# Optimization experiments

Measured on AMD Instinct MI355X. Metric: run time of the kernel, lower is better.

Reference implementation:

```python
import jax, jax.numpy as jnp
from jax import lax
import numpy as np

B, T, IN, H, OUT = 64, 512, 128, 512, 1


def _lstm_layer(x, W_ih, W_hh, b_ih, b_hh):
    # x: [B, T, in]; W_ih: [4H, in]; W_hh: [4H, H]; biases: [4H]
    # PyTorch gate order: i, f, g, o
    xg = jnp.einsum('bti,gi->btg', x, W_ih) + (b_ih + b_hh)  # [B, T, 4H]
    Hd = W_hh.shape[1]
    h0 = jnp.zeros((x.shape[0], Hd), x.dtype)

    def step(carry, xt):
        h, c = carry
        g = xt + h @ W_hh.T  # [B, 4H]
        i, f, gg, o = jnp.split(g, 4, axis=-1)
        i = jax.nn.sigmoid(i)
        f = jax.nn.sigmoid(f)
        gg = jnp.tanh(gg)
        o = jax.nn.sigmoid(o)
        c = f * c + i * gg
        h = o * jnp.tanh(c)
        return (h, c), h

    (_, _), hs = lax.scan(step, (h0, h0), jnp.swapaxes(xg, 0, 1))  # hs: [T, B, H]
    return jnp.swapaxes(hs, 0, 1)  # [B, T, H]


def setup_inputs() -> dict:
    key = jax.random.key(0)
    ks = jax.random.split(key, 11)
    s_in = 1.0 / np.sqrt(H)
    inp = {
        'x': jax.random.normal(ks[0], (B, T, IN), jnp.float32),
        'W_ih0': jax.random.uniform(ks[1], (4 * H, IN), jnp.float32, -s_in, s_in),
        'W_hh0': jax.random.uniform(ks[2], (4 * H, H), jnp.float32, -s_in, s_in),
        'b_ih0': jax.random.uniform(ks[3], (4 * H,), jnp.float32, -s_in, s_in),
        'b_hh0': jax.random.uniform(ks[4], (4 * H,), jnp.float32, -s_in, s_in),
        'W_ih1': jax.random.uniform(ks[5], (4 * H, H), jnp.float32, -s_in, s_in),
        'W_hh1': jax.random.uniform(ks[6], (4 * H, H), jnp.float32, -s_in, s_in),
        'b_ih1': jax.random.uniform(ks[7], (4 * H,), jnp.float32, -s_in, s_in),
        'b_hh1': jax.random.uniform(ks[8], (4 * H,), jnp.float32, -s_in, s_in),
        'Wl': jax.random.uniform(ks[9], (OUT, H), jnp.float32, -s_in, s_in),
        'bl': jax.random.uniform(ks[10], (OUT,), jnp.float32, -s_in, s_in),
    }
    return inp


def reference(x, W_ih0, W_hh0, b_ih0, b_hh0, W_ih1, W_hh1, b_ih1, b_hh1, Wl, bl):
    h = _lstm_layer(x, W_ih0, W_hh0, b_ih0, b_hh0)   # layer 0
    h = _lstm_layer(h, W_ih1, W_hh1, b_ih1, b_hh1)   # layer 1
    last = h[:, -1, :]                                # [B, H]
    out = last @ Wl.T + bl                            # [B, OUT]; classification=False -> no sigmoid
    return out
```

## Files before the change

### kernel.cpp

```cpp
#include <hip/hip_runtime.h>
#include <cmath>

#define TT 512
#define BB 64
#define HH 512
#define II 128
#define NBLK 256

typedef float v2f __attribute__((ext_vector_type(2)));
__device__ __forceinline__ v2f fma2(v2f a, v2f b, v2f c) { return __builtin_elementwise_fma(a, b, c); }

#define SMEM_FLOATS (16384 + 16384 + 1024 + 256 + 16)
#define SMEM_BYTES  (SMEM_FLOATS * 4)

__device__ __forceinline__ float sigm(float v) { return 1.0f / (1.0f + expf(-v)); }
__device__ __forceinline__ unsigned umin2(unsigned a, unsigned b) { return a < b ? a : b; }
#define CBAR() asm volatile("" ::: "memory")

__device__ __forceinline__ void step(const float* wk, float v, v2f (&acc)[8]) {
  const float4* wp = (const float4*)wk;
  const float4 w0 = wp[0], w1 = wp[1], w2 = wp[2], w3 = wp[3];
  const v2f vb = (v2f){v, v};
  acc[0] = fma2((v2f){w0.x, w0.y}, vb, acc[0]);
  acc[1] = fma2((v2f){w0.z, w0.w}, vb, acc[1]);
  acc[2] = fma2((v2f){w1.x, w1.y}, vb, acc[2]);
  acc[3] = fma2((v2f){w1.z, w1.w}, vb, acc[3]);
  acc[4] = fma2((v2f){w2.x, w2.y}, vb, acc[4]);
  acc[5] = fma2((v2f){w2.z, w2.w}, vb, acc[5]);
  acc[6] = fma2((v2f){w3.x, w3.y}, vb, acc[6]);
  acc[7] = fma2((v2f){w3.z, w3.w}, vb, acc[7]);
}

template<int KN>
__device__ __forceinline__ void loadva(const float* __restrict__ src, int k0,
                                       int b, float (&v)[KN]) {
#pragma unroll
  for (int i = 0; i < KN; ++i)
    v[i] = __hip_atomic_load(src + (size_t)(k0 + i) * BB + b,
                             __ATOMIC_RELAXED, __HIP_MEMORY_SCOPE_AGENT);
}
template<int KN>
__device__ __forceinline__ void loadv(const float* __restrict__ src, int k0,
                                      int b, float (&v)[KN]) {
#pragma unroll
  for (int i = 0; i < KN; ++i) v[i] = src[(size_t)(k0 + i) * BB + b];
}
template<int KN>
__device__ __forceinline__ void consume(const float* __restrict__ wbase, int k0,
                                        const float (&v)[KN], v2f (&acc)[8]) {
#pragma unroll
  for (int i = 0; i < KN; ++i) step(wbase + (size_t)(k0 + i) * 16, v[i], acc);
}

__device__ __forceinline__ void span32(const float* __restrict__ src,
                                       const float* __restrict__ wbase,
                                       int k0, int b, v2f (&acc)[8]) {
  float va[8], vb_[8];
  loadva<8>(src, k0, b, va);
  loadva<8>(src, k0 + 8, b, vb_);
  consume<8>(wbase, k0, va, acc);
  loadva<8>(src, k0 + 16, b, va);
  consume<8>(wbase, k0 + 8, vb_, acc);
  loadva<8>(src, k0 + 24, b, vb_);
  consume<8>(wbase, k0 + 16, va, acc);
  consume<8>(wbase, k0 + 24, vb_, acc);
}

__global__ __launch_bounds__(1024) void k_transpose_x(const float* __restrict__ x,
                                                      float* __restrict__ xT) {
  __shared__ float tile[64][65];
  const int t  = blockIdx.x >> 1;
  const int k0 = (blockIdx.x & 1) << 6;
  const int lk = threadIdx.x & 63;
  const int lb = threadIdx.x >> 6;
#pragma unroll
  for (int bp = 0; bp < 64; bp += 16) {
    const int b = bp + lb;
    tile[lk][b] = x[((size_t)b * TT + t) * II + k0 + lk];
  }
  __syncthreads();
  const int b2  = threadIdx.x & 63;
  const int kk0 = threadIdx.x >> 6;
#pragma unroll
  for (int kp = 0; kp < 64; kp += 16) {
    const int kk = kp + kk0;
    xT[((size_t)t * II + k0 + kk) * BB + b2] = tile[kk][b2];
  }
}

__global__ void k_init_flags(unsigned* flags) { flags[threadIdx.x] = 0u; }

__global__ __launch_bounds__(1024, 4) void k_lstm_persist(
    const float* __restrict__ xT,
    const float* __restrict__ W_ih0, const float* __restrict__ W_hh0,
    const float* __restrict__ b_ih0, const float* __restrict__ b_hh0,
    const float* __restrict__ W_ih1, const float* __restrict__ W_hh1,
    const float* __restrict__ b_ih1, const float* __restrict__ b_hh1,
    float* __restrict__ h0ring, float* __restrict__ h1ring,
    unsigned* __restrict__ flags)
{
  extern __shared__ float smem[];
  float* wlds  = smem;
  float* part  = wlds + 16384;
  float* gates = part + 16384;
  float* cst   = gates + 1024;
  float* bsum  = cst + 256;

  const int bid = blockIdx.x;
  const int L   = bid >> 7;
  const int ub  = (bid & 127) << 2;
  const int tid = threadIdx.x;

  const float* WA = L ? W_ih1 : W_ih0;
  const float* WB = L ? W_hh1 : W_hh0;
  const int KA = L ? HH : II;

  const int ktot = KA + HH;
  for (int idx = tid; idx < 16 * ktot; idx += 1024) {
    const int k  = idx >> 4;
    const int lr = idx & 15;
    const int u = lr >> 2, q = lr & 3;
    const int G = q * HH + ub + u;
    wlds[idx] = (k < KA) ? WA[G * KA + k] : WB[G * HH + (k - KA)];
  }
  if (tid < 16) {
    const int u = tid >> 2, q = tid & 3;
    const int G = q * HH + ub + u;
    bsum[tid] = L ? (b_ih1[G] + b_hh1[G]) : (b_ih0[G] + b_hh0[G]);
  }
  if (tid < 256) cst[tid] = 0.0f;
  __syncthreads();

  const int kseg = tid >> 6;
  const int b    = tid & 63;

  for (int s = 0; s <= TT; ++s) {
    const int t = L ? (s - 1) : s;
    const bool active = (t >= 0 && t < TT);
    const bool first  = (t == 0);

    v2f acc[8];
#pragma unroll
    for (int j = 0; j < 8; ++j) acc[j] = (v2f){0.0f, 0.0f};

    float xv[8];
    if (active && L == 0) {
      loadv<8>(xT + (size_t)t * (II * BB), kseg * 8, b, xv);
    }

    if (s > 0) {
      if (tid < 64) {
        const unsigned tgt = (unsigned)s;
        for (;;) {
          const unsigned m0 = __hip_atomic_load(flags + tid,       __ATOMIC_RELAXED, __HIP_MEMORY_SCOPE_AGENT);
          const unsigned m1 = __hip_atomic_load(flags + tid +  64, __ATOMIC_RELAXED, __HIP_MEMORY_SCOPE_AGENT);
          const unsigned m2 = __hip_atomic_load(flags + tid + 128, __ATOMIC_RELAXED, __HIP_MEMORY_SCOPE_AGENT);
          const unsigned m3 = __hip_atomic_load(flags + tid + 192, __ATOMIC_RELAXED, __HIP_MEMORY_SCOPE_AGENT);
          const unsigned mn = umin2(umin2(m0, m1), umin2(m2, m3));
          if (__all(mn >= tgt)) break;
          __builtin_amdgcn_s_sleep(1);
        }
      }
      __syncthreads();
      CBAR();
    }

    if (active) {
      if (L == 0) {
        consume<8>(wlds, kseg * 8, xv, acc);
        if (!first) {
          span32(h0ring + (size_t)((s - 1) & 1) * (HH * BB),
                 wlds + (size_t)II * 16, kseg * 32, b, acc);
        }
      } else {
        const float* h0p = h0ring + (size_t)((s - 1) & 1) * (HH * BB);
        span32(h0p, wlds, kseg * 32, b, acc);
        if (!first) {
          span32(h1ring + (size_t)(s & 1) * (HH * BB),
                 wlds + (size_t)HH * 16, kseg * 32, b, acc);
        }
      }

#pragma unroll
      for (int j = 0; j < 4; ++j) {
        part[(((j << 2) + 0) * 16 + kseg) * 64 + b] = acc[(j << 1)].x;
        part[(((j << 2) + 1) * 16 + kseg) * 64 + b] = acc[(j << 1)].y;
        part[(((j << 2) + 2) * 16 + kseg) * 64 + b] = acc[(j << 1) + 1].x;
        part[(((j << 2) + 3) * 16 + kseg) * 64 + b] = acc[(j << 1) + 1].y;
      }
      __syncthreads();
      {
        const int row = tid >> 6;
        const int bb  = tid & 63;
        float g = 0.0f;
#pragma unroll
        for (int ks = 0; ks < 16; ++ks) g += part[(row * 16 + ks) * 64 + bb];
        gates[row * 64 + bb] = g + bsum[row];
      }
      __syncthreads();

      if (tid < 256) {
        const int u = tid >> 6, bb = tid & 63;
        const float gi = sigm(gates[((u << 2) + 0) * 64 + bb]);
        const float gf = sigm(gates[((u << 2) + 1) * 64 + bb]);
        const float gg = tanhf(gates[((u << 2) + 2) * 64 + bb]);
        const float go = sigm(gates[((u << 2) + 3) * 64 + bb]);
        const float cold = first ? 0.0f : cst[u * 64 + bb];
        const float cn = gf * cold + gi * gg;
        const float hn = go * tanhf(cn);
        cst[u * 64 + bb] = cn;
        float* hdst = (L ? h1ring : h0ring) + (size_t)(t & 1) * (HH * BB);
        float old = __hip_atomic_exchange(hdst + (ub + u) * 64 + bb, hn,
                                          __ATOMIC_RELAXED, __HIP_MEMORY_SCOPE_AGENT);
        asm volatile("" :: "v"(old));
      }
    }

    __syncthreads();
    if (tid == 0) {
      __hip_atomic_store(flags + bid, (unsigned)(s + 1),
                         __ATOMIC_RELAXED, __HIP_MEMORY_SCOPE_AGENT);
    }
  }
}

__global__ __launch_bounds__(512) void k_final(const float* __restrict__ h1last,
                                               const float* __restrict__ Wl,
                                               const float* __restrict__ bl,
                                               float* __restrict__ out) {
  __shared__ float red[8][64];
  const int jg = threadIdx.x >> 6, b = threadIdx.x & 63;
  float a = 0.0f;
  for (int jj = 0; jj < 64; ++jj) {
    const int j = (jg << 6) + jj;
    a += h1last[j * BB + b] * Wl[j];
  }
  red[jg][b] = a;
  __syncthreads();
  if (threadIdx.x < 64) {
    float s = bl[0];
#pragma unroll
    for (int g = 0; g < 8; ++g) s += red[g][threadIdx.x];
    out[threadIdx.x] = s;
  }
}

extern "C" void kernel_launch(void* const* d_in, const int* in_sizes, int n_in,
                              void* d_out, int out_size, void* d_ws, size_t ws_size,
                              hipStream_t stream) {
  (void)in_sizes; (void)n_in; (void)out_size; (void)ws_size;
  const float* x     = (const float*)d_in[0];
  const float* W_ih0 = (const float*)d_in[1];
  const float* W_hh0 = (const float*)d_in[2];
  const float* b_ih0 = (const float*)d_in[3];
  const float* b_hh0 = (const float*)d_in[4];
  const float* W_ih1 = (const float*)d_in[5];
  const float* W_hh1 = (const float*)d_in[6];
  const float* b_ih1 = (const float*)d_in[7];
  const float* b_hh1 = (const float*)d_in[8];
  const float* Wl    = (const float*)d_in[9];
  const float* bl    = (const float*)d_in[10];
  float* out = (float*)d_out;

  float* ws       = (float*)d_ws;
  float* xT       = ws;
  float* h0ring   = xT + (size_t)TT * II * BB;
  float* h1ring   = h0ring + 2 * HH * BB;
  unsigned* flags = (unsigned*)(h1ring + 2 * HH * BB);

  k_transpose_x<<<1024, 1024, 0, stream>>>(x, xT);
  k_init_flags<<<1, NBLK, 0, stream>>>(flags);

  hipFuncSetAttribute((const void*)k_lstm_persist,
                      hipFuncAttributeMaxDynamicSharedMemorySize, SMEM_BYTES);

  void* args[] = {
    (void*)&xT,
    (void*)&W_ih0, (void*)&W_hh0, (void*)&b_ih0, (void*)&b_hh0,
    (void*)&W_ih1, (void*)&W_hh1, (void*)&b_ih1, (void*)&b_hh1,
    (void*)&h0ring, (void*)&h1ring, (void*)&flags,
  };
  hipLaunchCooperativeKernel((void*)k_lstm_persist, dim3(NBLK), dim3(1024),
                             args, SMEM_BYTES, stream);

  k_final<<<1, 512, 0, stream>>>(h1ring + HH * BB, Wl, bl, out);
}
```

Baseline: 7.520 ms.

## Decouple LSTM layer sync with per-layer flags and a deeper hidden-state ring

Replaces the single all-blocks-at-step-s barrier with separate flag arrays for layer 0 and layer 1. Layer 1 now runs two steps behind layer 0, and each layer waits on its own layer for step s but only on the other layer for step s-1. The hidden-state rings grow from 2 to 4 slots so that one step of slack between layers cannot overwrite data that is still being read. The aim is to let the two layers drift slightly, so a slow block in one layer does not stall the other every step. The cost is one extra pipeline step and a larger ring footprint.

```diff
diff --git a/kernel.cpp b/kernel.cpp
--- a/kernel.cpp
+++ b/kernel.cpp
@@ -6,6 +6,7 @@
 #define HH 512
 #define II 128
 #define NBLK 256
+#define RD 4
 
 typedef float v2f __attribute__((ext_vector_type(2)));
 __device__ __forceinline__ v2f fma2(v2f a, v2f b, v2f c) { return __builtin_elementwise_fma(a, b, c); }
@@ -97,7 +98,7 @@
     const float* __restrict__ W_ih1, const float* __restrict__ W_hh1,
     const float* __restrict__ b_ih1, const float* __restrict__ b_hh1,
     float* __restrict__ h0ring, float* __restrict__ h1ring,
-    unsigned* __restrict__ flags)
+    unsigned* __restrict__ flag0, unsigned* __restrict__ flag1)
 {
   extern __shared__ float smem[];
   float* wlds  = smem;
@@ -134,8 +135,10 @@
   const int kseg = tid >> 6;
   const int b    = tid & 63;
 
-  for (int s = 0; s <= TT; ++s) {
-    const int t = L ? (s - 1) : s;
+  const int SMAX = TT + 2;
+
+  for (int s = 0; s < SMAX; ++s) {
+    const int t = L ? (s - 2) : s;
     const bool active = (t >= 0 && t < TT);
     const bool first  = (t == 0);
 
@@ -150,14 +153,15 @@
 
     if (s > 0) {
       if (tid < 64) {
-        const unsigned tgt = (unsigned)s;
+        const unsigned tA = L ? (unsigned)(s - 1) : (unsigned)s;
+        const unsigned tB = L ? (unsigned)s : (unsigned)(s - 1);
         for (;;) {
-          const unsigned m0 = __hip_atomic_load(flags + tid,       __ATOMIC_RELAXED, __HIP_MEMORY_SCOPE_AGENT);
-          const unsigned m1 = __hip_atomic_load(flags + tid +  64, __ATOMIC_RELAXED, __HIP_MEMORY_SCOPE_AGENT);
-          const unsigned m2 = __hip_atomic_load(flags + tid + 128, __ATOMIC_RELAXED, __HIP_MEMORY_SCOPE_AGENT);
-          const unsigned m3 = __hip_atomic_load(flags + tid + 192, __ATOMIC_RELAXED, __HIP_MEMORY_SCOPE_AGENT);
-          const unsigned mn = umin2(umin2(m0, m1), umin2(m2, m3));
-          if (__all(mn >= tgt)) break;
+          const unsigned a0 = __hip_atomic_load(flag0 + tid,      __ATOMIC_RELAXED, __HIP_MEMORY_SCOPE_AGENT);
+          const unsigned a1 = __hip_atomic_load(flag0 + tid + 64, __ATOMIC_RELAXED, __HIP_MEMORY_SCOPE_AGENT);
+          const unsigned b0 = __hip_atomic_load(flag1 + tid,      __ATOMIC_RELAXED, __HIP_MEMORY_SCOPE_AGENT);
+          const unsigned b1 = __hip_atomic_load(flag1 + tid + 64, __ATOMIC_RELAXED, __HIP_MEMORY_SCOPE_AGENT);
+          const bool ok = (umin2(a0, a1) >= tA) && (umin2(b0, b1) >= tB);
+          if (__all(ok)) break;
           __builtin_amdgcn_s_sleep(1);
         }
       }
@@ -169,14 +173,14 @@
       if (L == 0) {
         consume<8>(wlds, kseg * 8, xv, acc);
         if (!first) {
-          span32(h0ring + (size_t)((s - 1) & 1) * (HH * BB),
+          span32(h0ring + (size_t)((s - 1) & 3) * (HH * BB),
                  wlds + (size_t)II * 16, kseg * 32, b, acc);
         }
       } else {
-        const float* h0p = h0ring + (size_t)((s - 1) & 1) * (HH * BB);
-        span32(h0p, wlds, kseg * 32, b, acc);
+        span32(h0ring + (size_t)((s - 2) & 3) * (HH * BB), wlds,
+               kseg * 32, b, acc);
         if (!first) {
-          span32(h1ring + (size_t)(s & 1) * (HH * BB),
+          span32(h1ring + (size_t)((s - 3) & 3) * (HH * BB),
                  wlds + (size_t)HH * 16, kseg * 32, b, acc);
         }
       }
@@ -209,7 +213,7 @@
         const float cn = gf * cold + gi * gg;
         const float hn = go * tanhf(cn);
         cst[u * 64 + bb] = cn;
-        float* hdst = (L ? h1ring : h0ring) + (size_t)(t & 1) * (HH * BB);
+        float* hdst = (L ? h1ring : h0ring) + (size_t)(t & 3) * (HH * BB);
         float old = __hip_atomic_exchange(hdst + (ub + u) * 64 + bb, hn,
                                           __ATOMIC_RELAXED, __HIP_MEMORY_SCOPE_AGENT);
         asm volatile("" :: "v"(old));
@@ -218,7 +222,8 @@
 
     __syncthreads();
     if (tid == 0) {
-      __hip_atomic_store(flags + bid, (unsigned)(s + 1),
+      unsigned* fl = (L ? flag1 : flag0) + (bid & 127);
+      __hip_atomic_store(fl, (unsigned)(s + 1),
                          __ATOMIC_RELAXED, __HIP_MEMORY_SCOPE_AGENT);
     }
   }
@@ -265,11 +270,12 @@
   float* ws       = (float*)d_ws;
   float* xT       = ws;
   float* h0ring   = xT + (size_t)TT * II * BB;
-  float* h1ring   = h0ring + 2 * HH * BB;
-  unsigned* flags = (unsigned*)(h1ring + 2 * HH * BB);
+  float* h1ring   = h0ring + (size_t)RD * HH * BB;
+  unsigned* flag0 = (unsigned*)(h1ring + (size_t)RD * HH * BB);
+  unsigned* flag1 = flag0 + 128;
 
   k_transpose_x<<<1024, 1024, 0, stream>>>(x, xT);
-  k_init_flags<<<1, NBLK, 0, stream>>>(flags);
+  k_init_flags<<<1, NBLK, 0, stream>>>(flag0);
 
   hipFuncSetAttribute((const void*)k_lstm_persist,
                       hipFuncAttributeMaxDynamicSharedMemorySize, SMEM_BYTES);
@@ -278,10 +284,11 @@
     (void*)&xT,
     (void*)&W_ih0, (void*)&W_hh0, (void*)&b_ih0, (void*)&b_hh0,
     (void*)&W_ih1, (void*)&W_hh1, (void*)&b_ih1, (void*)&b_hh1,
-    (void*)&h0ring, (void*)&h1ring, (void*)&flags,
+    (void*)&h0ring, (void*)&h1ring, (void*)&flag0, (void*)&flag1,
   };
   hipLaunchCooperativeKernel((void*)k_lstm_persist, dim3(NBLK), dim3(1024),
                              args, SMEM_BYTES, stream);
 
-  k_final<<<1, 512, 0, stream>>>(h1ring + HH * BB, Wl, bl, out);
-}
+  k_final<<<1, 512, 0, stream>>>(h1ring + (size_t)((TT - 1) & 3) * HH * BB,
+                                 Wl, bl, out);
+}
```

Measured after the change: 7.714 ms. +2.6%, slower.

## Stream pre-packed weights from global memory instead of staging them in LDS

Applied to the files above, without the earlier changes.

Adds a prep kernel that packs each block's gate weight slice into a contiguous global buffer. The persistent LSTM kernel then reads weights directly from global memory (uniform addresses, expected to be served by scalar/L2 caches) instead of copying them into LDS, which shrinks LDS use by 64KB per block. kseg is forced wave-uniform with readfirstlane so the weight loads can become scalar loads. The risk is that per-step weight reads now go to cache or global memory rather than LDS, which could add latency on the recurrent critical path.

```diff
diff --git a/kernel.cpp b/kernel.cpp
--- a/kernel.cpp
+++ b/kernel.cpp
@@ -10,7 +10,7 @@
 typedef float v2f __attribute__((ext_vector_type(2)));
 __device__ __forceinline__ v2f fma2(v2f a, v2f b, v2f c) { return __builtin_elementwise_fma(a, b, c); }
 
-#define SMEM_FLOATS (16384 + 16384 + 1024 + 256 + 16)
+#define SMEM_FLOATS (16384 + 1024 + 256 + 16)
 #define SMEM_BYTES  (SMEM_FLOATS * 4)
 
 __device__ __forceinline__ float sigm(float v) { return 1.0f / (1.0f + expf(-v)); }
@@ -88,20 +88,38 @@
   }
 }
 
+__global__ __launch_bounds__(1024) void k_prep_w(
+    const float* __restrict__ W_ih0, const float* __restrict__ W_hh0,
+    const float* __restrict__ W_ih1, const float* __restrict__ W_hh1,
+    float* __restrict__ wT) {
+  const int bid = blockIdx.x;
+  const int L   = bid >> 7;
+  const int ub  = (bid & 127) << 2;
+  const float* WA = L ? W_ih1 : W_ih0;
+  const float* WB = L ? W_hh1 : W_hh0;
+  const int KA = L ? HH : II;
+  const int ktot = KA + HH;
+  float* dst = wT + (size_t)bid * (16 * 1024);
+  for (int idx = threadIdx.x; idx < 16 * ktot; idx += 1024) {
+    const int k  = idx >> 4;
+    const int lr = idx & 15;
+    const int u = lr >> 2, q = lr & 3;
+    const int G = q * HH + ub + u;
+    dst[idx] = (k < KA) ? WA[G * KA + k] : WB[G * HH + (k - KA)];
+  }
+}
+
 __global__ void k_init_flags(unsigned* flags) { flags[threadIdx.x] = 0u; }
 
 __global__ __launch_bounds__(1024, 4) void k_lstm_persist(
-    const float* __restrict__ xT,
-    const float* __restrict__ W_ih0, const float* __restrict__ W_hh0,
+    const float* __restrict__ xT, const float* __restrict__ wT,
     const float* __restrict__ b_ih0, const float* __restrict__ b_hh0,
-    const float* __restrict__ W_ih1, const float* __restrict__ W_hh1,
     const float* __restrict__ b_ih1, const float* __restrict__ b_hh1,
     float* __restrict__ h0ring, float* __restrict__ h1ring,
     unsigned* __restrict__ flags)
 {
   extern __shared__ float smem[];
-  float* wlds  = smem;
-  float* part  = wlds + 16384;
+  float* part  = smem;
   float* gates = part + 16384;
   float* cst   = gates + 1024;
   float* bsum  = cst + 256;
@@ -110,19 +128,10 @@
   const int L   = bid >> 7;
   const int ub  = (bid & 127) << 2;
   const int tid = threadIdx.x;
-
-  const float* WA = L ? W_ih1 : W_ih0;
-  const float* WB = L ? W_hh1 : W_hh0;
-  const int KA = L ? HH : II;
-
-  const int ktot = KA + HH;
-  for (int idx = tid; idx < 16 * ktot; idx += 1024) {
-    const int k  = idx >> 4;
-    const int lr = idx & 15;
-    const int u = lr >> 2, q = lr & 3;
-    const int G = q * HH + ub + u;
-    wlds[idx] = (k < KA) ? WA[G * KA + k] : WB[G * HH + (k - KA)];
-  }
+  const int KA  = L ? HH : II;
+
+  const float* wblk = wT + (size_t)bid * (16 * 1024);
+
   if (tid < 16) {
     const int u = tid >> 2, q = tid & 3;
     const int G = q * HH + ub + u;
@@ -131,7 +140,7 @@
   if (tid < 256) cst[tid] = 0.0f;
   __syncthreads();
 
-  const int kseg = tid >> 6;
+  const int kseg = __builtin_amdgcn_readfirstlane(tid >> 6);
   const int b    = tid & 63;
 
   for (int s = 0; s <= TT; ++s) {
@@ -167,17 +176,17 @@
 
     if (active) {
       if (L == 0) {
-        consume<8>(wlds, kseg * 8, xv, acc);
+        consume<8>(wblk, kseg * 8, xv, acc);
         if (!first) {
           span32(h0ring + (size_t)((s - 1) & 1) * (HH * BB),
-                 wlds + (size_t)II * 16, kseg * 32, b, acc);
+                 wblk + (size_t)II * 16, kseg * 32, b, acc);
         }
       } else {
         const float* h0p = h0ring + (size_t)((s - 1) & 1) * (HH * BB);
-        span32(h0p, wlds, kseg * 32, b, acc);
+        span32(h0p, wblk, kseg * 32, b, acc);
         if (!first) {
           span32(h1ring + (size_t)(s & 1) * (HH * BB),
-                 wlds + (size_t)HH * 16, kseg * 32, b, acc);
+                 wblk + (size_t)HH * 16, kseg * 32, b, acc);
         }
       }
 
@@ -264,20 +273,21 @@
 
   float* ws       = (float*)d_ws;
   float* xT       = ws;
-  float* h0ring   = xT + (size_t)TT * II * BB;
+  float* wT       = xT + (size_t)TT * II * BB;
+  float* h0ring   = wT + (size_t)NBLK * 16 * 1024;
   float* h1ring   = h0ring + 2 * HH * BB;
   unsigned* flags = (unsigned*)(h1ring + 2 * HH * BB);
 
   k_transpose_x<<<1024, 1024, 0, stream>>>(x, xT);
+  k_prep_w<<<NBLK, 1024, 0, stream>>>(W_ih0, W_hh0, W_ih1, W_hh1, wT);
   k_init_flags<<<1, NBLK, 0, stream>>>(flags);
 
   hipFuncSetAttribute((const void*)k_lstm_persist,
                       hipFuncAttributeMaxDynamicSharedMemorySize, SMEM_BYTES);
 
   void* args[] = {
-    (void*)&xT,
-    (void*)&W_ih0, (void*)&W_hh0, (void*)&b_ih0, (void*)&b_hh0,
-    (void*)&W_ih1, (void*)&W_hh1, (void*)&b_ih1, (void*)&b_hh1,
+    (void*)&xT, (void*)&wT,
+    (void*)&b_ih0, (void*)&b_hh0, (void*)&b_ih1, (void*)&b_hh1,
     (void*)&h0ring, (void*)&h1ring, (void*)&flags,
   };
   hipLaunchCooperativeKernel((void*)k_lstm_persist, dim3(NBLK), dim3(1024),
```

New measurement: 9.907 ms. 1.32x slower.

## Use full-depth h rings with plain loads, pack h stores, overlap x consume

Applied to the files above, without the earlier changes.

When the workspace is large enough, the hidden-state rings get one slot per timestep. Each slot is then written exactly once, so reads can use ordinary cached loads instead of relaxed atomic loads, with an agent-scope acquire fence at kernel start. The pointwise gate stage now uses 128 threads, each handling two batch elements and writing both h values with a single 64-bit atomic exchange. Layer 0 also issues its h loads before consuming the x contribution so that load latency is hidden. The cost is a much larger workspace, and the correctness of plain loads depends on cache coherence across blocks on that hardware.

```diff
diff --git a/kernel.cpp b/kernel.cpp
--- a/kernel.cpp
+++ b/kernel.cpp
@@ -31,13 +31,17 @@
   acc[7] = fma2((v2f){w3.z, w3.w}, vb, acc[7]);
 }
 
-template<int KN>
-__device__ __forceinline__ void loadva(const float* __restrict__ src, int k0,
-                                       int b, float (&v)[KN]) {
-#pragma unroll
-  for (int i = 0; i < KN; ++i)
-    v[i] = __hip_atomic_load(src + (size_t)(k0 + i) * BB + b,
-                             __ATOMIC_RELAXED, __HIP_MEMORY_SCOPE_AGENT);
+template<bool DEEP, int KN>
+__device__ __forceinline__ void loadh(const float* __restrict__ src, int k0,
+                                      int b, float (&v)[KN]) {
+#pragma unroll
+  for (int i = 0; i < KN; ++i) {
+    if constexpr (DEEP)
+      v[i] = src[(size_t)(k0 + i) * BB + b];
+    else
+      v[i] = __hip_atomic_load(src + (size_t)(k0 + i) * BB + b,
+                               __ATOMIC_RELAXED, __HIP_MEMORY_SCOPE_AGENT);
+  }
 }
 template<int KN>
 __device__ __forceinline__ void loadv(const float* __restrict__ src, int k0,
@@ -52,16 +56,17 @@
   for (int i = 0; i < KN; ++i) step(wbase + (size_t)(k0 + i) * 16, v[i], acc);
 }
 
+template<bool DEEP>
 __device__ __forceinline__ void span32(const float* __restrict__ src,
                                        const float* __restrict__ wbase,
                                        int k0, int b, v2f (&acc)[8]) {
   float va[8], vb_[8];
-  loadva<8>(src, k0, b, va);
-  loadva<8>(src, k0 + 8, b, vb_);
+  loadh<DEEP, 8>(src, k0, b, va);
+  loadh<DEEP, 8>(src, k0 + 8, b, vb_);
   consume<8>(wbase, k0, va, acc);
-  loadva<8>(src, k0 + 16, b, va);
+  loadh<DEEP, 8>(src, k0 + 16, b, va);
   consume<8>(wbase, k0 + 8, vb_, acc);
-  loadva<8>(src, k0 + 24, b, vb_);
+  loadh<DEEP, 8>(src, k0 + 24, b, vb_);
   consume<8>(wbase, k0 + 16, va, acc);
   consume<8>(wbase, k0 + 24, vb_, acc);
 }
@@ -90,6 +95,7 @@
 
 __global__ void k_init_flags(unsigned* flags) { flags[threadIdx.x] = 0u; }
 
+template<bool DEEP>
 __global__ __launch_bounds__(1024, 4) void k_lstm_persist(
     const float* __restrict__ xT,
     const float* __restrict__ W_ih0, const float* __restrict__ W_hh0,
@@ -106,6 +112,8 @@
   float* cst   = gates + 1024;
   float* bsum  = cst + 256;
 
+  __builtin_amdgcn_fence(__ATOMIC_ACQUIRE, "agent");
+
   const int bid = blockIdx.x;
   const int L   = bid >> 7;
   const int ub  = (bid & 127) << 2;
@@ -138,6 +146,10 @@
     const int t = L ? (s - 1) : s;
     const bool active = (t >= 0 && t < TT);
     const bool first  = (t == 0);
+
+    const size_t sl_h0rd = DEEP ? (size_t)(s - 1) : (size_t)((s - 1) & 1);
+    const size_t sl_h1rd = DEEP ? (size_t)(s - 2) : (size_t)(s & 1);
+    const size_t sl_wr   = DEEP ? (size_t)t       : (size_t)(t & 1);
 
     v2f acc[8];
 #pragma unroll
@@ -167,17 +179,29 @@
 
     if (active) {
       if (L == 0) {
-        consume<8>(wlds, kseg * 8, xv, acc);
         if (!first) {
-          span32(h0ring + (size_t)((s - 1) & 1) * (HH * BB),
-                 wlds + (size_t)II * 16, kseg * 32, b, acc);
+          const float* src = h0ring + sl_h0rd * (HH * BB);
+          const float* wh  = wlds + (size_t)II * 16;
+          const int k0 = kseg * 32;
+          float va[8], vb_[8];
+          loadh<DEEP, 8>(src, k0, b, va);
+          loadh<DEEP, 8>(src, k0 + 8, b, vb_);
+          consume<8>(wlds, kseg * 8, xv, acc);
+          consume<8>(wh, k0, va, acc);
+          loadh<DEEP, 8>(src, k0 + 16, b, va);
+          consume<8>(wh, k0 + 8, vb_, acc);
+          loadh<DEEP, 8>(src, k0 + 24, b, vb_);
+          consume<8>(wh, k0 + 16, va, acc);
+          consume<8>(wh, k0 + 24, vb_, acc);
+        } else {
+          consume<8>(wlds, kseg * 8, xv, acc);
         }
       } else {
-        const float* h0p = h0ring + (size_t)((s - 1) & 1) * (HH * BB);
-        span32(h0p, wlds, kseg * 32, b, acc);
+        const float* h0p = h0ring + sl_h0rd * (HH * BB);
+        span32<DEEP>(h0p, wlds, kseg * 32, b, acc);
         if (!first) {
-          span32(h1ring + (size_t)(s & 1) * (HH * BB),
-                 wlds + (size_t)HH * 16, kseg * 32, b, acc);
+          span32<DEEP>(h1ring + sl_h1rd * (HH * BB),
+                       wlds + (size_t)HH * 16, kseg * 32, b, acc);
         }
       }
 
@@ -199,25 +223,38 @@
       }
       __syncthreads();
 
-      if (tid < 256) {
-        const int u = tid >> 6, bb = tid & 63;
-        const float gi = sigm(gates[((u << 2) + 0) * 64 + bb]);
-        const float gf = sigm(gates[((u << 2) + 1) * 64 + bb]);
-        const float gg = tanhf(gates[((u << 2) + 2) * 64 + bb]);
-        const float go = sigm(gates[((u << 2) + 3) * 64 + bb]);
-        const float cold = first ? 0.0f : cst[u * 64 + bb];
-        const float cn = gf * cold + gi * gg;
-        const float hn = go * tanhf(cn);
-        cst[u * 64 + bb] = cn;
-        float* hdst = (L ? h1ring : h0ring) + (size_t)(t & 1) * (HH * BB);
-        float old = __hip_atomic_exchange(hdst + (ub + u) * 64 + bb, hn,
-                                          __ATOMIC_RELAXED, __HIP_MEMORY_SCOPE_AGENT);
+      if (tid < 128) {
+        const int u   = tid >> 5;
+        const int bb0 = (tid & 31) << 1, bb1 = bb0 + 1;
+        const float gi0 = sigm(gates[((u << 2) + 0) * 64 + bb0]);
+        const float gf0 = sigm(gates[((u << 2) + 1) * 64 + bb0]);
+        const float gg0 = tanhf(gates[((u << 2) + 2) * 64 + bb0]);
+        const float go0 = sigm(gates[((u << 2) + 3) * 64 + bb0]);
+        const float gi1 = sigm(gates[((u << 2) + 0) * 64 + bb1]);
+        const float gf1 = sigm(gates[((u << 2) + 1) * 64 + bb1]);
+        const float gg1 = tanhf(gates[((u << 2) + 2) * 64 + bb1]);
+        const float go1 = sigm(gates[((u << 2) + 3) * 64 + bb1]);
+        const float c0 = first ? 0.0f : cst[u * 64 + bb0];
+        const float c1 = first ? 0.0f : cst[u * 64 + bb1];
+        const float cn0 = gf0 * c0 + gi0 * gg0;
+        const float cn1 = gf1 * c1 + gi1 * gg1;
+        const float hn0 = go0 * tanhf(cn0);
+        const float hn1 = go1 * tanhf(cn1);
+        cst[u * 64 + bb0] = cn0;
+        cst[u * 64 + bb1] = cn1;
+        float* hdst = (L ? h1ring : h0ring) + sl_wr * (HH * BB);
+        unsigned long long pk =
+            (unsigned long long)__float_as_uint(hn0) |
+            ((unsigned long long)__float_as_uint(hn1) << 32);
+        unsigned long long old = __hip_atomic_exchange(
+            (unsigned long long*)(hdst + (ub + u) * 64 + bb0), pk,
+            __ATOMIC_RELAXED, __HIP_MEMORY_SCOPE_AGENT);
         asm volatile("" :: "v"(old));
       }
     }
 
     __syncthreads();
-    if (tid == 0) {
+    if (tid == 0 && s < TT) {
       __hip_atomic_store(flags + bid, (unsigned)(s + 1),
                          __ATOMIC_RELAXED, __HIP_MEMORY_SCOPE_AGENT);
     }
@@ -248,7 +285,7 @@
 extern "C" void kernel_launch(void* const* d_in, const int* in_sizes, int n_in,
                               void* d_out, int out_size, void* d_ws, size_t ws_size,
                               hipStream_t stream) {
-  (void)in_sizes; (void)n_in; (void)out_size; (void)ws_size;
+  (void)in_sizes; (void)n_in; (void)out_size;
   const float* x     = (const float*)d_in[0];
   const float* W_ih0 = (const float*)d_in[1];
   const float* W_hh0 = (const float*)d_in[2];
@@ -262,17 +299,23 @@
   const float* bl    = (const float*)d_in[10];
   float* out = (float*)d_out;
 
+  const size_t xt_f   = (size_t)TT * II * BB;
+  const size_t ring_f = (size_t)(TT + 1) * HH * BB;
+  const size_t need   = (xt_f + 2 * ring_f) * 4 + 4096;
+  const bool deep = (ws_size >= need);
+  const size_t rslots = deep ? (size_t)(TT + 1) : 2;
+
   float* ws       = (float*)d_ws;
   float* xT       = ws;
-  float* h0ring   = xT + (size_t)TT * II * BB;
-  float* h1ring   = h0ring + 2 * HH * BB;
-  unsigned* flags = (unsigned*)(h1ring + 2 * HH * BB);
+  float* h0ring   = xT + xt_f;
+  float* h1ring   = h0ring + rslots * HH * BB;
+  unsigned* flags = (unsigned*)(h1ring + rslots * HH * BB);
 
   k_transpose_x<<<1024, 1024, 0, stream>>>(x, xT);
   k_init_flags<<<1, NBLK, 0, stream>>>(flags);
 
-  hipFuncSetAttribute((const void*)k_lstm_persist,
-                      hipFuncAttributeMaxDynamicSharedMemorySize, SMEM_BYTES);
+  void* fn = deep ? (void*)k_lstm_persist<true> : (void*)k_lstm_persist<false>;
+  hipFuncSetAttribute(fn, hipFuncAttributeMaxDynamicSharedMemorySize, SMEM_BYTES);
 
   void* args[] = {
     (void*)&xT,
@@ -280,8 +323,8 @@
     (void*)&W_ih1, (void*)&W_hh1, (void*)&b_ih1, (void*)&b_hh1,
     (void*)&h0ring, (void*)&h1ring, (void*)&flags,
   };
-  hipLaunchCooperativeKernel((void*)k_lstm_persist, dim3(NBLK), dim3(1024),
-                             args, SMEM_BYTES, stream);
-
-  k_final<<<1, 512, 0, stream>>>(h1ring + HH * BB, Wl, bl, out);
-}
+  hipLaunchCooperativeKernel(fn, dim3(NBLK), dim3(1024), args, SMEM_BYTES, stream);
+
+  float* h1last = h1ring + (deep ? (size_t)(TT - 1) : (size_t)1) * HH * BB;
+  k_final<<<1, 512, 0, stream>>>(h1last, Wl, bl, out);
+}
```

Measured after the change: 7.860 ms. +4.5%, slower.
